# Performance work log

Hardware: AMD Instinct MI355X
Metric: run time of the kernel (lower is better)

Reference implementation:

```python
import jax, jax.numpy as jnp
import numpy as np

CHANNEL_DIM = 256
RATE = 4
KSIZE = 2 * RATE - 1  # odd=True


def bilinear_kernel(size, normalize=False):
    factor = (size + 1) // 2
    center = factor - 1 if size % 2 == 1 else factor - 0.5
    og = np.ogrid[:size, :size]
    kern = (1 - abs(og[0] - center) / factor) * (1 - abs(og[1] - center) / factor)
    if normalize:
        kern = kern / kern.sum()
    return kern.astype(np.float32)


def setup_inputs() -> dict:
    key = jax.random.key(0)
    x = jax.random.normal(key, (4, CHANNEL_DIM, 64, 64), dtype=jnp.float32)
    # The torch module builds a [C, C, k, k] weight that is block-diagonal:
    # weight[c, c] = bilinear kernel, all cross-channel blocks are zero.
    # We store only the nonzero diagonal as a depthwise kernel [C, 1, k, k]
    # (OIHW with feature_group_count=C), which computes identical math.
    kern = jnp.asarray(bilinear_kernel(KSIZE, normalize=False))  # [k, k]
    weight = jnp.broadcast_to(kern[None, None], (CHANNEL_DIM, 1, KSIZE, KSIZE))
    return {"x": x, "weight": weight}


def reference(x, weight):
    # F.conv_transpose2d(x, W, stride=r) with no padding/output_padding is
    # equivalent to a cross-correlation of the input dilated by r (lhs_dilation)
    # with the spatially-flipped kernel and padding k-1 on each side.
    # The bilinear kernel is symmetric, so the flip is a no-op.
    k = weight.shape[-1]
    return jax.lax.conv_general_dilated(
        x, weight,
        window_strides=(1, 1),
        padding=((k - 1, k - 1), (k - 1, k - 1)),
        lhs_dilation=(RATE, RATE),
        dimension_numbers=("NCHW", "OIHW", "NCHW"),
        feature_group_count=CHANNEL_DIM,
    )  # -> [N, C, (H-1)*rate + k, (W-1)*rate + k] = [4, 256, 259, 259]
```

## Files before the change

kernel.cpp:

```cpp
#include <hip/hip_runtime.h>


#define IH 64
#define IW 64
#define OH 259
#define OW 259
#define NC 1024

__global__ __launch_bounds__(256) void upsample4x_rows(
    const float* __restrict__ x, float* __restrict__ out)
{
    const int qy   = blockIdx.x;
    const int nc   = blockIdx.y;
    const int py   = threadIdx.x >> 6;
    const int lane = threadIdx.x & 63;

    const int oy = 4 * qy + py;
    if (oy >= OH) return;

    float wyl = 0.25f * (float)(3 - py);
    float wyh = 0.25f * (float)(py + 1);
    int iyl = qy - 1;
    int iyh = qy;
    if (iyl < 0)      { iyl = 0;      wyl = 0.0f; }
    if (iyh > IH - 1) { iyh = IH - 1; wyh = 0.0f; }

    const float* __restrict__ xp = x + (size_t)nc * (IH * IW);
    float xl = xp[iyl * IW + lane];
    float xh = xp[iyh * IW + lane];
    float v0 = wyl * xl + wyh * xh;

    float vm1 = __shfl_up(v0, 1);
    float vp1 = __shfl_down(v0, 1);
    if (lane == 0)  vm1 = 0.0f;
    if (lane == 63) vp1 = 0.0f;

    const size_t row_off = (size_t)nc * (OH * OW) + (size_t)oy * OW;
    const int s = (int)((4 - (row_off & 3)) & 3);

    float e0, e1, e2, e3;
    {
        float e[4];
#pragma unroll
        for (int j = 0; j < 4; ++j) {
            int sj = s + j;
            int c  = sj >> 2;
            int px = sj & 3;
            float wl = 0.25f * (float)(3 - px);
            float wh = 0.25f * (float)(px + 1);
            float lo = c ? v0  : vm1;
            float hi = c ? vp1 : v0;
            e[j] = wl * lo + wh * hi;
        }
        e0 = e[0]; e1 = e[1]; e2 = e[2]; e3 = e[3];
    }
    float4* dst = (float4*)(out + row_off + s);
    dst[lane] = make_float4(e0, e1, e2, e3);

    if (lane == 0) {
        for (int ox = 0; ox < s; ++ox)
            out[row_off + ox] = 0.25f * (float)(ox + 1) * v0;
    }
    if (lane == 63) {
        for (int ox = s + 256; ox < OW; ++ox)
            out[row_off + ox] = 0.25f * (float)(3 - (ox & 3)) * v0;
    }
}

extern "C" void kernel_launch(void* const* d_in, const int* in_sizes, int n_in,
                              void* d_out, int out_size, void* d_ws, size_t ws_size,
                              hipStream_t stream)
{
    const float* x = (const float*)d_in[0];
    float* out = (float*)d_out;

    dim3 grid(65, NC);
    dim3 block(256);
    upsample4x_rows<<<grid, block, 0, stream>>>(x, out);
}
```

Before: 314.4 us.

## Process 8-row input strips per wave with register-carried input rows

Each wavefront now handles one strip of eight input rows for one channel and walks down it, carrying the previous and current input rows and their horizontal neighbours in registers. This replaces one block per quad of output rows, which reloaded two input rows per wave. Alignment offsets and blend weights are precomputed per sub-row phase. The aim is fewer redundant loads and less launch and block overhead on a write-bound kernel. The cost is far fewer waves (2048 blocks versus about 66k) and serial per-wave loops, which may reduce memory-level parallelism.

```diff
diff --git a/kernel.cpp b/kernel.cpp
--- a/kernel.cpp
+++ b/kernel.cpp
@@ -5,65 +5,88 @@
 #define IW 64
 #define OH 259
 #define OW 259
-#define NC 1024
+#define OROW 67081
 
-__global__ __launch_bounds__(256) void upsample4x_rows(
+__global__ __launch_bounds__(256) void upsample4x_strip(
     const float* __restrict__ x, float* __restrict__ out)
 {
-    const int qy   = blockIdx.x;
-    const int nc   = blockIdx.y;
-    const int py   = threadIdx.x >> 6;
+    const int wv   = threadIdx.x >> 6;
     const int lane = threadIdx.x & 63;
+    const int g    = blockIdx.x * 4 + wv;
+    const int strip = g & 7;
+    const int nc    = g >> 3;
 
-    const int oy = 4 * qy + py;
-    if (oy >= OH) return;
-
-    float wyl = 0.25f * (float)(3 - py);
-    float wyh = 0.25f * (float)(py + 1);
-    int iyl = qy - 1;
-    int iyh = qy;
-    if (iyl < 0)      { iyl = 0;      wyl = 0.0f; }
-    if (iyh > IH - 1) { iyh = IH - 1; wyh = 0.0f; }
+    const int q0 = strip * 8;
+    const int q1 = (strip == 7) ? 65 : q0 + 8;
 
     const float* __restrict__ xp = x + (size_t)nc * (IH * IW);
-    float xl = xp[iyl * IW + lane];
-    float xh = xp[iyh * IW + lane];
-    float v0 = wyl * xl + wyh * xh;
+    const size_t out_base = (size_t)nc * OROW;
 
-    float vm1 = __shfl_up(v0, 1);
-    float vp1 = __shfl_down(v0, 1);
-    if (lane == 0)  vm1 = 0.0f;
-    if (lane == 63) vp1 = 0.0f;
-
-    const size_t row_off = (size_t)nc * (OH * OW) + (size_t)oy * OW;
-    const int s = (int)((4 - (row_off & 3)) & 3);
-
-    float e0, e1, e2, e3;
-    {
-        float e[4];
+    float wl_t[4][4], wh_t[4][4];
+    int   c_t[4][4];
+    int   s_t[4];
+#pragma unroll
+    for (int py = 0; py < 4; ++py) {
+        int s = (4 - ((nc + 3 * py) & 3)) & 3;
+        s_t[py] = s;
 #pragma unroll
         for (int j = 0; j < 4; ++j) {
             int sj = s + j;
-            int c  = sj >> 2;
-            int px = sj & 3;
-            float wl = 0.25f * (float)(3 - px);
-            float wh = 0.25f * (float)(px + 1);
-            float lo = c ? v0  : vm1;
-            float hi = c ? vp1 : v0;
-            e[j] = wl * lo + wh * hi;
+            c_t[py][j]  = sj >> 2;
+            int px      = sj & 3;
+            wl_t[py][j] = 0.25f * (float)(3 - px);
+            wh_t[py][j] = 0.25f * (float)(px + 1);
         }
-        e0 = e[0]; e1 = e[1]; e2 = e[2]; e3 = e[3];
     }
-    float4* dst = (float4*)(out + row_off + s);
-    dst[lane] = make_float4(e0, e1, e2, e3);
 
-    if (lane == 0) {
-        for (int ox = 0; ox < s; ++ox)
-            out[row_off + ox] = 0.25f * (float)(ox + 1) * v0;
-    }
-    if (lane == 63) {
-        for (int ox = s + 256; ox < OW; ++ox)
-            out[row_off + ox] = 0.25f * (float)(3 - (ox & 3)) * v0;
+    float xl = (q0 == 0) ? 0.0f : xp[(q0 - 1) * IW + lane];
+    float xh = xp[q0 * IW + lane];
+    float xlm = __shfl_up(xl, 1);   if (lane == 0)  xlm = 0.0f;
+    float xlp = __shfl_down(xl, 1); if (lane == 63) xlp = 0.0f;
+    float xhm = __shfl_up(xh, 1);   if (lane == 0)  xhm = 0.0f;
+    float xhp = __shfl_down(xh, 1); if (lane == 63) xhp = 0.0f;
+
+    for (int q = q0; q < q1; ++q) {
+        int qn = q + 1;
+        float xn = 0.0f;
+        if (qn < q1 && qn <= IH - 1) xn = xp[qn * IW + lane];
+
+#pragma unroll
+        for (int py = 0; py < 4; ++py) {
+            int oy = 4 * q + py;
+            if (oy < OH) {
+                float wyl = 0.25f * (float)(3 - py);
+                float wyh = 0.25f * (float)(py + 1);
+                float v0  = wyl * xl  + wyh * xh;
+                float vm1 = wyl * xlm + wyh * xhm;
+                float vp1 = wyl * xlp + wyh * xhp;
+
+                const int s = s_t[py];
+                float e[4];
+#pragma unroll
+                for (int j = 0; j < 4; ++j) {
+                    float lo = c_t[py][j] ? v0  : vm1;
+                    float hi = c_t[py][j] ? vp1 : v0;
+                    e[j] = wl_t[py][j] * lo + wh_t[py][j] * hi;
+                }
+
+                const size_t row = out_base + (size_t)oy * OW;
+                float4* dst = (float4*)(out + row + s);
+                dst[lane] = make_float4(e[0], e[1], e[2], e[3]);
+
+                if (lane == 0)
+                    for (int ox = 0; ox < s; ++ox)
+                        out[row + ox] = 0.25f * (float)(ox + 1) * v0;
+                if (lane == 63)
+                    for (int ox = s + 256; ox < OW; ++ox)
+                        out[row + ox] = 0.25f * (float)(3 - (ox & 3)) * v0;
+            }
+        }
+
+        xl = xh; xlm = xhm; xlp = xhp;
+        xh = xn;
+        xhm = __shfl_up(xh, 1);   if (lane == 0)  xhm = 0.0f;
+        xhp = __shfl_down(xh, 1); if (lane == 63) xhp = 0.0f;
     }
 }
 
@@ -74,7 +97,5 @@
     const float* x = (const float*)d_in[0];
     float* out = (float*)d_out;
 
-    dim3 grid(65, NC);
-    dim3 block(256);
-    upsample4x_rows<<<grid, block, 0, stream>>>(x, out);
+    upsample4x_strip<<<2048, 256, 0, stream>>>(x, out);
 }
```

After: 310.3 us. About the same (-1.3%).
